# Kernel tuning notes

Hardware: AMD Instinct MI355X
Metric: run time of the kernel (lower is better)

## Reference

```python
import jax, jax.numpy as jnp
import numpy as np

SAMPLES = 16        # samples per spatial dim -> M = SAMPLES**2 sample points
SAMPLE_PAD = 0
K = 9               # nearest neighbors == conv kernel size == stride


def setup_inputs() -> dict:
    key = jax.random.key(0)
    k1, k2, k3 = jax.random.split(key, 3)
    B, C, H, W = 16, 128, 64, 64
    OUT = 128
    x = jax.random.normal(k1, (B, C, H, W), dtype=jnp.float32)
    w = jax.random.normal(k2, (OUT, C, K), dtype=jnp.float32) * 0.05
    b = jax.random.normal(k3, (OUT,), dtype=jnp.float32) * 0.05
    return {"x": x, "w": w, "b": b}


def reference(x, w, b):
    B, C, H, W = x.shape
    N = H * W
    # --- spatial sample grid (static, shape-derived) ---
    xi = jnp.round(jnp.linspace(SAMPLE_PAD, H - SAMPLE_PAD - 1, SAMPLES)).astype(jnp.int32)
    yi = jnp.round(jnp.linspace(SAMPLE_PAD, W - SAMPLE_PAD - 1, SAMPLES)).astype(jnp.int32)
    xg, yg = jnp.meshgrid(xi, yi, indexing='ij')
    x_sample = x[:, :, xg, yg].reshape(B, C, -1)          # (B, C, M)
    x1 = x.reshape(B, C, N)                                # (B, C, N)
    # --- squared Euclidean distance between tokens and samples ---
    dots = jnp.einsum('bcn,bcm->bnm', x1, x_sample)        # (B, N, M)
    n2 = jnp.sum(x1 * x1, axis=1)                          # (B, N)
    m2 = jnp.sum(x_sample * x_sample, axis=1)              # (B, M)
    dist2 = n2[:, :, None] + m2[:, None, :] - 2.0 * dots   # (B, N, M)
    # K nearest samples per token (smallest distance)
    _, idx = jax.lax.top_k(-dist2, K)                      # (B, N, K) int32
    # gather neighbor features from the sample set: (B, C, N, K)
    nbrs = jnp.take_along_axis(x_sample[:, :, None, :],
                               idx[:, None, :, :], axis=3)
    # Conv1d(kernel=K, stride=K) over the (B, C, N*K) prime tensor
    out = jnp.einsum('bcnk,ock->bon', nbrs, w) + b[None, :, None]
    return out.reshape(B, w.shape[0], H, W)
```

## Files before the change

### kernel.cpp

```cpp
#include <hip/hip_runtime.h>

#define NB   16
#define NC   128
#define NN   4096
#define NM   256
#define NK   9
#define NO   128

#define DELTA 0.03f

typedef __attribute__((ext_vector_type(8))) short bf16x8;
typedef __attribute__((ext_vector_type(4))) float f32x4;

__device__ __constant__ int d_grid16[16] = {0,4,8,13,17,21,25,29,34,38,42,46,50,55,59,63};

__device__ inline unsigned short bf16_rne(float v) {
    unsigned u = __float_as_uint(v);
    return (unsigned short)((u + 0x7FFFu + ((u >> 16) & 1u)) >> 16);
}

__global__ __launch_bounds__(256) void k_prep(const float* __restrict__ x,
                                              const float* __restrict__ w,
                                              float* __restrict__ xs,
                                              float* __restrict__ xsT,
                                              unsigned short* __restrict__ xsTh,
                                              unsigned short* __restrict__ xsTl,
                                              float* __restrict__ Wr) {
    __shared__ float tile[16 * 260];
    int bx = blockIdx.x, t = threadIdx.x;
    if (bx < 128) {
        int b = bx >> 3, c0 = (bx & 7) * 16;
        int m = t;
        int pix = d_grid16[m >> 4] * 64 + d_grid16[m & 15];
        #pragma unroll
        for (int cc = 0; cc < 16; ++cc) {
            float v = x[((size_t)b * NC + c0 + cc) * NN + pix];
            xs[((size_t)b * NC + c0 + cc) * NM + m] = v;
            tile[cc * 260 + m] = v;
        }
        __syncthreads();
        #pragma unroll
        for (int e = 0; e < 4; ++e) {
            float fv[4];
            fv[0] = tile[(4 * e + 0) * 260 + m];
            fv[1] = tile[(4 * e + 1) * 260 + m];
            fv[2] = tile[(4 * e + 2) * 260 + m];
            fv[3] = tile[(4 * e + 3) * 260 + m];
            size_t base = ((size_t)b * NM + m) * NC + c0 + 4 * e;
            *(float4*)&xsT[base] = make_float4(fv[0], fv[1], fv[2], fv[3]);
            unsigned short h4[4], l4[4];
            #pragma unroll
            for (int e2 = 0; e2 < 4; ++e2) {
                unsigned short h = bf16_rne(fv[e2]);
                h4[e2] = h;
                l4[e2] = bf16_rne(fv[e2] - __uint_as_float(((unsigned)h) << 16));
            }
            *(ushort4*)&xsTh[base] = make_ushort4(h4[0], h4[1], h4[2], h4[3]);
            *(ushort4*)&xsTl[base] = make_ushort4(l4[0], l4[1], l4[2], l4[3]);
        }
    } else {
        int f = (bx - 128) * 256 + t;
        int o = f & 127;
        int k = (f >> 7) % 9;
        int c = f / 1152;
        Wr[f] = w[o * 1152 + c * 9 + k];
    }
}

__global__ __launch_bounds__(256) void k_g(const float* __restrict__ xs,
                                           const float* __restrict__ Wr,
                                           const float* __restrict__ xsT,
                                           float* __restrict__ G,
                                           float* __restrict__ m2) {
    __shared__ float xsl[64 * 64];
    __shared__ float wl[64 * 128];
    int t = threadIdx.x;
    if (blockIdx.z == 16) {
        #pragma clang fp contract(off)
        int fl = blockIdx.x * 4 + blockIdx.y;
        if (fl < 16) {
            const float* p = xsT + ((size_t)fl * NM + t) * NC;
            float a = 0.f;
            for (int c4 = 0; c4 < 32; ++c4) {
                float4 v = *(const float4*)&p[4 * c4];
                a = __fadd_rn(a, __fmul_rn(v.x, v.x));
                a = __fadd_rn(a, __fmul_rn(v.y, v.y));
                a = __fadd_rn(a, __fmul_rn(v.z, v.z));
                a = __fadd_rn(a, __fmul_rn(v.w, v.w));
            }
            m2[fl * NM + t] = a;
        }
        return;
    }
    int kk = blockIdx.x, mt = blockIdx.y, b = blockIdx.z;
    int to = t & 31, tmm = t >> 5;
    float acc[8][4] = {};
    for (int c0 = 0; c0 < NC; c0 += 64) {
        __syncthreads();
        #pragma unroll
        for (int it = 0; it < 16; ++it) {
            int f = it * 256 + t;
            int cc = f >> 6, mm = f & 63;
            xsl[f] = xs[((size_t)b * NC + c0 + cc) * NM + mt * 64 + mm];
        }
        #pragma unroll
        for (int it = 0; it < 32; ++it) {
            int f = it * 256 + t;
            int cc = f >> 7, o = f & 127;
            wl[f] = Wr[(size_t)(c0 + cc) * 1152 + kk * 128 + o];
        }
        __syncthreads();
        for (int cc = 0; cc < 64; ++cc) {
            const float4 a0 = *(const float4*)&xsl[cc * 64 + tmm * 8];
            const float4 a1 = *(const float4*)&xsl[cc * 64 + tmm * 8 + 4];
            float av[8] = {a0.x, a0.y, a0.z, a0.w, a1.x, a1.y, a1.z, a1.w};
            float2 w0 = *(const float2*)&wl[cc * 128 + 2 * to];
            float2 w1 = *(const float2*)&wl[cc * 128 + 64 + 2 * to];
            float wv[4] = {w0.x, w0.y, w1.x, w1.y};
            #pragma unroll
            for (int i = 0; i < 8; ++i)
                #pragma unroll
                for (int j = 0; j < 4; ++j)
                    acc[i][j] = fmaf(av[i], wv[j], acc[i][j]);
        }
    }
    #pragma unroll
    for (int i = 0; i < 8; ++i) {
        size_t base = (((size_t)(b * NM + mt * 64 + tmm * 8 + i) * NK + kk) << 7);
        *(float2*)&G[base + 2 * to]      = make_float2(acc[i][0], acc[i][1]);
        *(float2*)&G[base + 64 + 2 * to] = make_float2(acc[i][2], acc[i][3]);
    }
}

__global__ __launch_bounds__(256, 4) void k_selref(const float* __restrict__ x,
                                                   const unsigned short* __restrict__ xsTh,
                                                   const unsigned short* __restrict__ xsTl,
                                                   const float* __restrict__ xsT,
                                                   const float* __restrict__ m2,
                                                   int* __restrict__ idx) {
    #pragma clang fp contract(off)
    __shared__ float x1l[128 * 33];
    __shared__ unsigned keysl[16 * 256];
    __shared__ float m2l[256];
    __shared__ int cntl[32];
    __shared__ unsigned short candl[32 * 16];
    __shared__ unsigned long long pairs[32 * 17];
    int b = blockIdx.y, n0 = blockIdx.x * 32;
    int t = threadIdx.x;
    int w = t >> 6, lane = t & 63;
    int lr = lane & 15, quad = lane >> 4;
    m2l[t] = m2[b * NM + t];
    if (t < 32) cntl[t] = 0;
    #pragma unroll
    for (int it = 0; it < 4; ++it) {
        int f4 = it * 256 + t;
        int c = f4 >> 3, nn4 = (f4 & 7) * 4;
        float4 v = *(const float4*)&x[((size_t)b * NC + c) * NN + n0 + nn4];
        *(float4*)&x1l[c * 33 + nn4] = v;
    }
    __syncthreads();
    f32x4 acc[2][4];
    #pragma unroll
    for (int i = 0; i < 2; ++i)
        #pragma unroll
        for (int j = 0; j < 4; ++j) acc[i][j] = (f32x4){0.f, 0.f, 0.f, 0.f};
    for (int kb = 0; kb < 4; ++kb) {
        bf16x8 Ah[2], Al[2];
        #pragma unroll
        for (int i = 0; i < 2; ++i) {
            unsigned short h8[8], l8[8];
            #pragma unroll
            for (int e = 0; e < 8; ++e) {
                float v = x1l[(kb * 32 + quad * 8 + e) * 33 + 16 * i + lr];
                unsigned short h = bf16_rne(v);
                h8[e] = h;
                l8[e] = bf16_rne(v - __uint_as_float(((unsigned)h) << 16));
            }
            Ah[i] = *(bf16x8*)h8;
            Al[i] = *(bf16x8*)l8;
        }
        bf16x8 bh[4], bl[4];
        #pragma unroll
        for (int j = 0; j < 4; ++j)
            bh[j] = *(const bf16x8*)&xsTh[((size_t)b * NM + 64 * w + 16 * j + lr) * NC + kb * 32 + quad * 8];
        #pragma unroll
        for (int i = 0; i < 2; ++i)
            #pragma unroll
            for (int j = 0; j < 4; ++j)
                acc[i][j] = __builtin_amdgcn_mfma_f32_16x16x32_bf16(Ah[i], bh[j], acc[i][j], 0, 0, 0);
        #pragma unroll
        for (int i = 0; i < 2; ++i)
            #pragma unroll
            for (int j = 0; j < 4; ++j)
                acc[i][j] = __builtin_amdgcn_mfma_f32_16x16x32_bf16(Al[i], bh[j], acc[i][j], 0, 0, 0);
        #pragma unroll
        for (int j = 0; j < 4; ++j)
            bl[j] = *(const bf16x8*)&xsTl[((size_t)b * NM + 64 * w + 16 * j + lr) * NC + kb * 32 + quad * 8];
        #pragma unroll
        for (int i = 0; i < 2; ++i)
            #pragma unroll
            for (int j = 0; j < 4; ++j)
                acc[i][j] = __builtin_amdgcn_mfma_f32_16x16x32_bf16(Ah[i], bl[j], acc[i][j], 0, 0, 0);
    }
    for (int h = 0; h < 2; ++h) {
        __syncthreads();
        #pragma unroll
        for (int r = 0; r < 4; ++r) {
            int tokL = 4 * quad + r;
            #pragma unroll
            for (int j = 0; j < 4; ++j) {
                int m = 64 * w + 16 * j + lr;
                float key = fmaf(-2.f, acc[h][j][r], m2l[m]);
                unsigned u = __float_as_uint(key);
                u = (u & 0x80000000u) ? ~u : (u | 0x80000000u);
                keysl[tokL * 256 + ((m + 8 * tokL) & 255)] = u;
            }
        }
        __syncthreads();
        int tokL = t >> 4, q = t & 15;
        unsigned bk[9];
        #pragma unroll
        for (int j = 0; j < 9; ++j) bk[j] = 0xFFFFFFFFu;
        #pragma unroll
        for (int s = 0; s < 16; ++s) {
            int col = (16 * s + q + 8 * tokL) & 255;
            unsigned v = keysl[tokL * 256 + col];
            #pragma unroll
            for (int j = 0; j < 9; ++j) {
                unsigned mn = min(v, bk[j]);
                v = max(v, bk[j]);
                bk[j] = mn;
            }
        }
        #pragma unroll
        for (int d = 1; d <= 8; d <<= 1) {
            unsigned pv[9];
            #pragma unroll
            for (int j = 0; j < 9; ++j) pv[j] = (unsigned)__shfl_xor((int)bk[j], d, 64);
            #pragma unroll
            for (int j = 0; j < 9; ++j) {
                unsigned v = pv[j];
                if (v >= bk[8]) break;
                #pragma unroll
                for (int jj = 0; jj < 9; ++jj) {
                    unsigned mn = min(v, bk[jj]);
                    v = max(v, bk[jj]);
                    bk[jj] = mn;
                }
            }
        }
        unsigned u9 = bk[8];
        unsigned ku = (u9 & 0x80000000u) ? (u9 & 0x7FFFFFFFu) : ~u9;
        float thf = __uint_as_float(ku) + DELTA;
        unsigned tu = __float_as_uint(thf);
        tu = (tu & 0x80000000u) ? ~tu : (tu | 0x80000000u);
        int tok = 16 * h + tokL;
        #pragma unroll
        for (int s = 0; s < 16; ++s) {
            int col = (16 * s + q + 8 * tokL) & 255;
            unsigned v = keysl[tokL * 256 + col];
            if (v <= tu) {
                int pos = atomicAdd(&cntl[tok], 1);
                if (pos < 16) candl[tok * 16 + pos] = (unsigned short)((col - 8 * tokL) & 255);
            }
        }
    }
    __syncthreads();
    if (t < 32) {
        int c = min(cntl[t], 16);
        for (int s = c; s < 16; ++s) candl[t * 16 + s] = 0xFFFFu;
    }
    __syncthreads();
    {
        int tok = t >> 3, q8 = t & 7;
        float n2 = 0.f;
        #pragma unroll 4
        for (int c = 0; c < NC; ++c) {
            float v = x1l[c * 33 + tok];
            n2 = __fadd_rn(n2, __fmul_rn(v, v));
        }
        int mym[2];
        unsigned long long myp[2];
        #pragma unroll
        for (int s = 0; s < 2; ++s) {
            int slot = q8 + 8 * s;
            int m = candl[tok * 16 + slot];
            mym[s] = m;
            unsigned long long p = ~0ull;
            if (m != 0xFFFF) {
                const float* xt = xsT + ((size_t)b * NM + m) * NC;
                float dot = 0.f;
                for (int c4 = 0; c4 < 32; ++c4) {
                    float4 sv = *(const float4*)&xt[4 * c4];
                    dot = __fadd_rn(dot, __fmul_rn(x1l[(4 * c4 + 0) * 33 + tok], sv.x));
                    dot = __fadd_rn(dot, __fmul_rn(x1l[(4 * c4 + 1) * 33 + tok], sv.y));
                    dot = __fadd_rn(dot, __fmul_rn(x1l[(4 * c4 + 2) * 33 + tok], sv.z));
                    dot = __fadd_rn(dot, __fmul_rn(x1l[(4 * c4 + 3) * 33 + tok], sv.w));
                }
                float key = __fsub_rn(__fadd_rn(n2, m2l[m]), __fmul_rn(2.f, dot));
                unsigned u = __float_as_uint(key);
                u = (u & 0x80000000u) ? ~u : (u | 0x80000000u);
                p = ((unsigned long long)u << 32) | (unsigned)m;
            }
            myp[s] = p;
            pairs[tok * 17 + slot] = p;
        }
        __syncthreads();
        unsigned long long pl[16];
        #pragma unroll
        for (int l2 = 0; l2 < 16; ++l2) pl[l2] = pairs[tok * 17 + l2];
        size_t obase = (size_t)(b * NN + n0 + tok) * NK;
        #pragma unroll
        for (int s = 0; s < 2; ++s) {
            if (mym[s] != 0xFFFF) {
                int rank = 0;
                #pragma unroll
                for (int l2 = 0; l2 < 16; ++l2) rank += (pl[l2] < myp[s]);
                if (rank < 9) idx[obase + rank] = mym[s];
            }
        }
    }
}

__global__ __launch_bounds__(256) void k_out(const float* __restrict__ G,
                                             const int* __restrict__ idx,
                                             const float* __restrict__ bias,
                                             float* __restrict__ out) {
    __shared__ float S[64 * 129];
    __shared__ int   idxl[576];
    __shared__ float biasl[128];
    int b = blockIdx.y, n0 = blockIdx.x * 64;
    int t = threadIdx.x;
    if (t < 128) biasl[t] = bias[t];
    for (int f = t; f < 576; f += 256) idxl[f] = idx[(size_t)(b * NN + n0) * NK + f];
    __syncthreads();
    int o = t & 127, half = t >> 7;
    for (int p = 0; p < 32; ++p) {
        int n = p * 2 + half;
        float a = biasl[o];
        #pragma unroll
        for (int k = 0; k < 9; ++k) {
            int m = idxl[n * 9 + k];
            a += G[(((size_t)(b * NM + m)) * NK + k) * 128 + o];
        }
        S[n * 129 + o] = a;
    }
    __syncthreads();
    int nn = t & 63, ob = t >> 6;
    for (int p = 0; p < 32; ++p) {
        int o2 = p * 4 + ob;
        out[((size_t)(b * NO + o2)) * NN + n0 + nn] = S[nn * 129 + o2];
    }
}

extern "C" void kernel_launch(void* const* d_in, const int* in_sizes, int n_in,
                              void* d_out, int out_size, void* d_ws, size_t ws_size,
                              hipStream_t stream) {
    const float* x    = (const float*)d_in[0];
    const float* w    = (const float*)d_in[1];
    const float* bias = (const float*)d_in[2];
    float* out = (float*)d_out;

    float* ws   = (float*)d_ws;
    float* m2   = ws;
    float* xs   = ws + 4096;
    float* xsT  = ws + 528384;
    float* Wr   = ws + 1052672;
    float* G    = ws + 1200128;
    int*   idx  = (int*)(ws + 5918720);
    unsigned short* xsTh = (unsigned short*)(ws + 6508544);
    unsigned short* xsTl = (unsigned short*)(ws + 6770688);

    k_prep  <<<dim3(704),       dim3(256), 0, stream>>>(x, w, xs, xsT, xsTh, xsTl, Wr);
    k_g     <<<dim3(9, 4, 17),  dim3(256), 0, stream>>>(xs, Wr, xsT, G, m2);
    k_selref<<<dim3(128, 16),   dim3(256), 0, stream>>>(x, xsTh, xsTl, xsT, m2, idx);
    k_out   <<<dim3(64, 16),    dim3(256), 0, stream>>>(G, idx, bias, out);
}
```

Measured before the change: 236.5 us.

## Use split-bf16 MFMA for G, precompute norms in prep, transpose token tile

The fp32 FMA GEMM that builds the per-sample weight products G is replaced by a split-precision bf16 MFMA version (hi/lo pairs, three products). The weights are pre-split into bf16 hi/lo in the prep kernel. Token and sample squared norms also move into prep, so the selection kernel no longer recomputes n2. The selection kernel's shared token tile becomes token-major, allowing float4 loads. Grids are flattened with batch in the low bits, and the redundant xs copy and the separate pairs buffer are dropped. Split-bf16 G trades some accuracy relative to fp32.

```diff
diff --git a/kernel.cpp b/kernel.cpp
--- a/kernel.cpp
+++ b/kernel.cpp
@@ -21,11 +21,13 @@
 
 __global__ __launch_bounds__(256) void k_prep(const float* __restrict__ x,
                                               const float* __restrict__ w,
-                                              float* __restrict__ xs,
                                               float* __restrict__ xsT,
                                               unsigned short* __restrict__ xsTh,
                                               unsigned short* __restrict__ xsTl,
-                                              float* __restrict__ Wr) {
+                                              unsigned short* __restrict__ Wth,
+                                              unsigned short* __restrict__ Wtl,
+                                              float* __restrict__ n2g,
+                                              float* __restrict__ m2) {
     __shared__ float tile[16 * 260];
     int bx = blockIdx.x, t = threadIdx.x;
     if (bx < 128) {
@@ -33,11 +35,8 @@
         int m = t;
         int pix = d_grid16[m >> 4] * 64 + d_grid16[m & 15];
         #pragma unroll
-        for (int cc = 0; cc < 16; ++cc) {
-            float v = x[((size_t)b * NC + c0 + cc) * NN + pix];
-            xs[((size_t)b * NC + c0 + cc) * NM + m] = v;
-            tile[cc * 260 + m] = v;
-        }
+        for (int cc = 0; cc < 16; ++cc)
+            tile[cc * 260 + m] = x[((size_t)b * NC + c0 + cc) * NN + pix];
         __syncthreads();
         #pragma unroll
         for (int e = 0; e < 4; ++e) {
@@ -58,78 +57,73 @@
             *(ushort4*)&xsTh[base] = make_ushort4(h4[0], h4[1], h4[2], h4[3]);
             *(ushort4*)&xsTl[base] = make_ushort4(l4[0], l4[1], l4[2], l4[3]);
         }
+    } else if (bx < 704) {
+        int f = (bx - 128) * 256 + t;
+        int ko = f >> 7, c = f & 127;
+        int o = ko & 127, k = ko >> 7;
+        float v = w[(size_t)o * 1152 + c * 9 + k];
+        unsigned short h = bf16_rne(v);
+        Wth[f] = h;
+        Wtl[f] = bf16_rne(v - __uint_as_float(((unsigned)h) << 16));
+    } else if (bx < 960) {
+        #pragma clang fp contract(off)
+        int i = bx - 704;
+        int b = i >> 4, n = (i & 15) * 256 + t;
+        const float* p = x + (size_t)b * NC * NN + n;
+        float a = 0.f;
+        #pragma unroll 4
+        for (int c = 0; c < NC; ++c) { float v = p[(size_t)c * NN]; a = __fadd_rn(a, __fmul_rn(v, v)); }
+        n2g[(size_t)b * NN + n] = a;
     } else {
-        int f = (bx - 128) * 256 + t;
-        int o = f & 127;
-        int k = (f >> 7) % 9;
-        int c = f / 1152;
-        Wr[f] = w[o * 1152 + c * 9 + k];
-    }
-}
-
-__global__ __launch_bounds__(256) void k_g(const float* __restrict__ xs,
-                                           const float* __restrict__ Wr,
-                                           const float* __restrict__ xsT,
-                                           float* __restrict__ G,
-                                           float* __restrict__ m2) {
-    __shared__ float xsl[64 * 64];
-    __shared__ float wl[64 * 128];
+        #pragma clang fp contract(off)
+        int b = bx - 960;
+        int pix = d_grid16[t >> 4] * 64 + d_grid16[t & 15];
+        const float* p = x + (size_t)b * NC * NN + pix;
+        float a = 0.f;
+        #pragma unroll 4
+        for (int c = 0; c < NC; ++c) { float v = p[(size_t)c * NN]; a = __fadd_rn(a, __fmul_rn(v, v)); }
+        m2[b * NM + t] = a;
+    }
+}
+
+__global__ __launch_bounds__(256) void k_g(const unsigned short* __restrict__ xsTh,
+                                           const unsigned short* __restrict__ xsTl,
+                                           const unsigned short* __restrict__ Wth,
+                                           const unsigned short* __restrict__ Wtl,
+                                           float* __restrict__ G) {
+    int id = blockIdx.x;
+    int b = id & 15, r = id >> 4;
+    int kk = r % 9, mt = r / 9;
     int t = threadIdx.x;
-    if (blockIdx.z == 16) {
-        #pragma clang fp contract(off)
-        int fl = blockIdx.x * 4 + blockIdx.y;
-        if (fl < 16) {
-            const float* p = xsT + ((size_t)fl * NM + t) * NC;
-            float a = 0.f;
-            for (int c4 = 0; c4 < 32; ++c4) {
-                float4 v = *(const float4*)&p[4 * c4];
-                a = __fadd_rn(a, __fmul_rn(v.x, v.x));
-                a = __fadd_rn(a, __fmul_rn(v.y, v.y));
-                a = __fadd_rn(a, __fmul_rn(v.z, v.z));
-                a = __fadd_rn(a, __fmul_rn(v.w, v.w));
-            }
-            m2[fl * NM + t] = a;
-        }
-        return;
-    }
-    int kk = blockIdx.x, mt = blockIdx.y, b = blockIdx.z;
-    int to = t & 31, tmm = t >> 5;
-    float acc[8][4] = {};
-    for (int c0 = 0; c0 < NC; c0 += 64) {
-        __syncthreads();
-        #pragma unroll
-        for (int it = 0; it < 16; ++it) {
-            int f = it * 256 + t;
-            int cc = f >> 6, mm = f & 63;
-            xsl[f] = xs[((size_t)b * NC + c0 + cc) * NM + mt * 64 + mm];
-        }
-        #pragma unroll
-        for (int it = 0; it < 32; ++it) {
-            int f = it * 256 + t;
-            int cc = f >> 7, o = f & 127;
-            wl[f] = Wr[(size_t)(c0 + cc) * 1152 + kk * 128 + o];
-        }
-        __syncthreads();
-        for (int cc = 0; cc < 64; ++cc) {
-            const float4 a0 = *(const float4*)&xsl[cc * 64 + tmm * 8];
-            const float4 a1 = *(const float4*)&xsl[cc * 64 + tmm * 8 + 4];
-            float av[8] = {a0.x, a0.y, a0.z, a0.w, a1.x, a1.y, a1.z, a1.w};
-            float2 w0 = *(const float2*)&wl[cc * 128 + 2 * to];
-            float2 w1 = *(const float2*)&wl[cc * 128 + 64 + 2 * to];
-            float wv[4] = {w0.x, w0.y, w1.x, w1.y};
-            #pragma unroll
-            for (int i = 0; i < 8; ++i)
-                #pragma unroll
-                for (int j = 0; j < 4; ++j)
-                    acc[i][j] = fmaf(av[i], wv[j], acc[i][j]);
-        }
-    }
-    #pragma unroll
-    for (int i = 0; i < 8; ++i) {
-        size_t base = (((size_t)(b * NM + mt * 64 + tmm * 8 + i) * NK + kk) << 7);
-        *(float2*)&G[base + 2 * to]      = make_float2(acc[i][0], acc[i][1]);
-        *(float2*)&G[base + 64 + 2 * to] = make_float2(acc[i][2], acc[i][3]);
-    }
+    int w = t >> 6, lane = t & 63;
+    int lr = lane & 15, quad = lane >> 4;
+    int m = b * NM + mt * 64 + w * 16 + lr;
+    const unsigned short* aph = xsTh + (size_t)m * NC;
+    const unsigned short* apl = xsTl + (size_t)m * NC;
+    f32x4 acc[8];
+    #pragma unroll
+    for (int j = 0; j < 8; ++j) acc[j] = (f32x4){0.f, 0.f, 0.f, 0.f};
+    #pragma unroll
+    for (int kb = 0; kb < 4; ++kb) {
+        int co = kb * 32 + quad * 8;
+        bf16x8 Ah = *(const bf16x8*)&aph[co];
+        bf16x8 Al = *(const bf16x8*)&apl[co];
+        #pragma unroll
+        for (int j = 0; j < 8; ++j) {
+            size_t wrow = ((size_t)kk * 128 + 16 * j + lr) * NC + co;
+            bf16x8 Bh = *(const bf16x8*)&Wth[wrow];
+            bf16x8 Bl = *(const bf16x8*)&Wtl[wrow];
+            acc[j] = __builtin_amdgcn_mfma_f32_16x16x32_bf16(Ah, Bh, acc[j], 0, 0, 0);
+            acc[j] = __builtin_amdgcn_mfma_f32_16x16x32_bf16(Al, Bh, acc[j], 0, 0, 0);
+            acc[j] = __builtin_amdgcn_mfma_f32_16x16x32_bf16(Ah, Bl, acc[j], 0, 0, 0);
+        }
+    }
+    int mrow = b * NM + mt * 64 + w * 16 + quad * 4;
+    #pragma unroll
+    for (int j = 0; j < 8; ++j)
+        #pragma unroll
+        for (int r2 = 0; r2 < 4; ++r2)
+            G[((size_t)(mrow + r2)) * 1152 + kk * 128 + 16 * j + lr] = acc[j][r2];
 }
 
 __global__ __launch_bounds__(256, 4) void k_selref(const float* __restrict__ x,
@@ -137,26 +131,31 @@
                                                    const unsigned short* __restrict__ xsTl,
                                                    const float* __restrict__ xsT,
                                                    const float* __restrict__ m2,
+                                                   const float* __restrict__ n2g,
                                                    int* __restrict__ idx) {
     #pragma clang fp contract(off)
-    __shared__ float x1l[128 * 33];
-    __shared__ unsigned keysl[16 * 256];
+    __shared__ __align__(16) float x1l[32 * 132];
+    __shared__ __align__(16) unsigned keysl[16 * 256];
     __shared__ float m2l[256];
+    __shared__ float n2l[32];
     __shared__ int cntl[32];
     __shared__ unsigned short candl[32 * 16];
-    __shared__ unsigned long long pairs[32 * 17];
-    int b = blockIdx.y, n0 = blockIdx.x * 32;
+    unsigned long long* pairs = (unsigned long long*)keysl;
+    int b = blockIdx.x & 15, n0 = (blockIdx.x >> 4) * 32;
     int t = threadIdx.x;
     int w = t >> 6, lane = t & 63;
     int lr = lane & 15, quad = lane >> 4;
     m2l[t] = m2[b * NM + t];
-    if (t < 32) cntl[t] = 0;
+    if (t < 32) { n2l[t] = n2g[(size_t)b * NN + n0 + t]; cntl[t] = 0; }
     #pragma unroll
     for (int it = 0; it < 4; ++it) {
         int f4 = it * 256 + t;
         int c = f4 >> 3, nn4 = (f4 & 7) * 4;
         float4 v = *(const float4*)&x[((size_t)b * NC + c) * NN + n0 + nn4];
-        *(float4*)&x1l[c * 33 + nn4] = v;
+        x1l[(nn4 + 0) * 132 + c] = v.x;
+        x1l[(nn4 + 1) * 132 + c] = v.y;
+        x1l[(nn4 + 2) * 132 + c] = v.z;
+        x1l[(nn4 + 3) * 132 + c] = v.w;
     }
     __syncthreads();
     f32x4 acc[2][4];
@@ -168,13 +167,15 @@
         bf16x8 Ah[2], Al[2];
         #pragma unroll
         for (int i = 0; i < 2; ++i) {
+            const float4 va = *(const float4*)&x1l[(16 * i + lr) * 132 + kb * 32 + quad * 8];
+            const float4 vb = *(const float4*)&x1l[(16 * i + lr) * 132 + kb * 32 + quad * 8 + 4];
+            float vf[8] = {va.x, va.y, va.z, va.w, vb.x, vb.y, vb.z, vb.w};
             unsigned short h8[8], l8[8];
             #pragma unroll
             for (int e = 0; e < 8; ++e) {
-                float v = x1l[(kb * 32 + quad * 8 + e) * 33 + 16 * i + lr];
-                unsigned short h = bf16_rne(v);
+                unsigned short h = bf16_rne(vf[e]);
                 h8[e] = h;
-                l8[e] = bf16_rne(v - __uint_as_float(((unsigned)h) << 16));
+                l8[e] = bf16_rne(vf[e] - __uint_as_float(((unsigned)h) << 16));
             }
             Ah[i] = *(bf16x8*)h8;
             Al[i] = *(bf16x8*)l8;
@@ -273,29 +274,24 @@
     __syncthreads();
     {
         int tok = t >> 3, q8 = t & 7;
-        float n2 = 0.f;
-        #pragma unroll 4
-        for (int c = 0; c < NC; ++c) {
-            float v = x1l[c * 33 + tok];
-            n2 = __fadd_rn(n2, __fmul_rn(v, v));
-        }
+        float n2 = n2l[tok];
         int mym[2];
         unsigned long long myp[2];
         #pragma unroll
         for (int s = 0; s < 2; ++s) {
-            int slot = q8 + 8 * s;
-            int m = candl[tok * 16 + slot];
+            int m = candl[tok * 16 + q8 + 8 * s];
             mym[s] = m;
             unsigned long long p = ~0ull;
             if (m != 0xFFFF) {
                 const float* xt = xsT + ((size_t)b * NM + m) * NC;
                 float dot = 0.f;
                 for (int c4 = 0; c4 < 32; ++c4) {
+                    float4 xv = *(const float4*)&x1l[tok * 132 + 4 * c4];
                     float4 sv = *(const float4*)&xt[4 * c4];
-                    dot = __fadd_rn(dot, __fmul_rn(x1l[(4 * c4 + 0) * 33 + tok], sv.x));
-                    dot = __fadd_rn(dot, __fmul_rn(x1l[(4 * c4 + 1) * 33 + tok], sv.y));
-                    dot = __fadd_rn(dot, __fmul_rn(x1l[(4 * c4 + 2) * 33 + tok], sv.z));
-                    dot = __fadd_rn(dot, __fmul_rn(x1l[(4 * c4 + 3) * 33 + tok], sv.w));
+                    dot = __fadd_rn(dot, __fmul_rn(xv.x, sv.x));
+                    dot = __fadd_rn(dot, __fmul_rn(xv.y, sv.y));
+                    dot = __fadd_rn(dot, __fmul_rn(xv.z, sv.z));
+                    dot = __fadd_rn(dot, __fmul_rn(xv.w, sv.w));
                 }
                 float key = __fsub_rn(__fadd_rn(n2, m2l[m]), __fmul_rn(2.f, dot));
                 unsigned u = __float_as_uint(key);
@@ -303,7 +299,7 @@
                 p = ((unsigned long long)u << 32) | (unsigned)m;
             }
             myp[s] = p;
-            pairs[tok * 17 + slot] = p;
+            pairs[tok * 17 + q8 + 8 * s] = p;
         }
         __syncthreads();
         unsigned long long pl[16];
@@ -329,7 +325,7 @@
     __shared__ float S[64 * 129];
     __shared__ int   idxl[576];
     __shared__ float biasl[128];
-    int b = blockIdx.y, n0 = blockIdx.x * 64;
+    int b = blockIdx.x & 15, n0 = (blockIdx.x >> 4) * 64;
     int t = threadIdx.x;
     if (t < 128) biasl[t] = bias[t];
     for (int f = t; f < 576; f += 256) idxl[f] = idx[(size_t)(b * NN + n0) * NK + f];
@@ -363,16 +359,17 @@
 
     float* ws   = (float*)d_ws;
     float* m2   = ws;
-    float* xs   = ws + 4096;
-    float* xsT  = ws + 528384;
-    float* Wr   = ws + 1052672;
-    float* G    = ws + 1200128;
-    int*   idx  = (int*)(ws + 5918720);
-    unsigned short* xsTh = (unsigned short*)(ws + 6508544);
-    unsigned short* xsTl = (unsigned short*)(ws + 6770688);
-
-    k_prep  <<<dim3(704),       dim3(256), 0, stream>>>(x, w, xs, xsT, xsTh, xsTl, Wr);
-    k_g     <<<dim3(9, 4, 17),  dim3(256), 0, stream>>>(xs, Wr, xsT, G, m2);
-    k_selref<<<dim3(128, 16),   dim3(256), 0, stream>>>(x, xsTh, xsTl, xsT, m2, idx);
-    k_out   <<<dim3(64, 16),    dim3(256), 0, stream>>>(G, idx, bias, out);
-}
+    float* n2g  = ws + 4096;
+    float* xsT  = ws + 69632;
+    float* G    = ws + 593920;
+    int*   idx  = (int*)(ws + 5312512);
+    unsigned short* xsTh = (unsigned short*)(ws + 5902336);
+    unsigned short* xsTl = (unsigned short*)(ws + 6164480);
+    unsigned short* Wth  = (unsigned short*)(ws + 6426624);
+    unsigned short* Wtl  = (unsigned short*)(ws + 6500352);
+
+    k_prep  <<<dim3(976),  dim3(256), 0, stream>>>(x, w, xsT, xsTh, xsTl, Wth, Wtl, n2g, m2);
+    k_g     <<<dim3(576),  dim3(256), 0, stream>>>(xsTh, xsTl, Wth, Wtl, G);
+    k_selref<<<dim3(2048), dim3(256), 0, stream>>>(x, xsTh, xsTl, xsT, m2, n2g, idx);
+    k_out   <<<dim3(1024), dim3(256), 0, stream>>>(G, idx, bias, out);
+}
```

New measurement: 227.6 us. 1.04x faster.
